# Performance work log

Measured on AMD Instinct MI355X. Metric: run time of the kernel, lower is better.

Reference implementation:

```python
import jax, jax.numpy as jnp
import numpy as np

HIDDEN_DIM = 256
N = 8192


def setup_inputs() -> dict:
    key = jax.random.key(0)
    k1, k2, k3, k4 = jax.random.split(key, 4)
    img = jax.random.normal(k1, (N, HIDDEN_DIM), dtype=jnp.float32)
    text = jax.random.normal(k2, (N, HIDDEN_DIM), dtype=jnp.float32)
    # nn.Linear(hidden_dim, hidden_dim, bias=False) weights, shape [out, in]
    scale = 1.0 / np.sqrt(HIDDEN_DIM)
    Wq = jax.random.uniform(k3, (HIDDEN_DIM, HIDDEN_DIM), dtype=jnp.float32, minval=-scale, maxval=scale)
    Wk = jax.random.uniform(k4, (HIDDEN_DIM, HIDDEN_DIM), dtype=jnp.float32, minval=-scale, maxval=scale)
    return {"img": img, "text": text, "Wq": Wq, "Wk": Wk}


def reference(img, text, Wq, Wk):
    d = img.shape[-1]
    norm_fact = 1.0 / jnp.sqrt(jnp.asarray(d, dtype=img.dtype))
    Q = img @ Wq.T                       # [N, D]
    K = text @ Wk.T                      # [N, D]
    scores = Q @ K.T                     # [N, N]
    # softmax over dim=1 (keys), then scaled by 1/sqrt(D)
    attn = jax.nn.softmax(scores, axis=1) * norm_fact
    out_img = attn @ img                 # [N, D]
    out_text = attn @ text               # [N, D]
    return (out_img, out_text)
```

## Files before the change

### kernel.cpp

```cpp
#include <hip/hip_runtime.h>

typedef unsigned short ushort_t;
typedef unsigned int uint_t;
typedef __attribute__((ext_vector_type(8))) short short8;
typedef __attribute__((ext_vector_type(8))) _Float16 half8;
typedef __attribute__((ext_vector_type(4))) _Float16 half4;
typedef __attribute__((ext_vector_type(4))) float float4v;

#define MFMA_BF16(a, b, c) __builtin_amdgcn_mfma_f32_16x16x32_bf16((a), (b), (c), 0, 0, 0)
#define MFMA_F16(a, b, c) __builtin_amdgcn_mfma_f32_16x16x32_f16((a), (b), (c), 0, 0, 0)

#define NQ 8192
#define DIM 256
#define DV 512

__device__ __forceinline__ ushort_t f2bf(float x) {
  union { float f; uint_t u; } v; v.f = x;
  return (ushort_t)((v.u + 0x7fffu + ((v.u >> 16) & 1u)) >> 16);
}
__device__ __forceinline__ float bf2f(ushort_t b) {
  union { uint_t u; float f; } v; v.u = ((uint_t)b) << 16;
  return v.f;
}

__device__ __forceinline__ half8 cvt8h(const float* p) {
  float4v a = *(const float4v*)p;
  float4v b = *(const float4v*)(p + 4);
  half8 r;
  r[0] = (_Float16)a[0]; r[1] = (_Float16)a[1];
  r[2] = (_Float16)a[2]; r[3] = (_Float16)a[3];
  r[4] = (_Float16)b[0]; r[5] = (_Float16)b[1];
  r[6] = (_Float16)b[2]; r[7] = (_Float16)b[3];
  return r;
}

__device__ __forceinline__ half8 as_h8(short8 s) {
  union { short8 s; half8 h; } u; u.s = s; return u.h;
}

__device__ __forceinline__ void load_lds_16(const void* g, void* l) {
  __builtin_amdgcn_global_load_lds(
      (const __attribute__((address_space(1))) uint_t*)g,
      (__attribute__((address_space(3))) uint_t*)l, 16, 0, 0);
}

__device__ __forceinline__ void barrier_vm0_lgkm0() {
  asm volatile("s_waitcnt vmcnt(0) lgkmcnt(0)\ns_barrier" ::: "memory");
}
__device__ __forceinline__ void barrier_lgkm0() {
  asm volatile("s_waitcnt lgkmcnt(0)\ns_barrier" ::: "memory");
}

__global__ __launch_bounds__(256, 2) void pre_kernel(
    const float* __restrict__ img, const float* __restrict__ text,
    const float* __restrict__ Wq, const float* __restrict__ Wk,
    _Float16* __restrict__ Qh, _Float16* __restrict__ Kh,
    ushort_t* __restrict__ Vt) {
  __shared__ float tile[64][65];
  const int bid = blockIdx.x;
  const int tid = threadIdx.x;
  if (bid < 1024) {
    const int bx = bid & 127;
    const int by = (bid >> 7) & 3;
    const int bz = bid >> 9;
    const int lane = tid & 63;
    const int wv = tid >> 6;
    const int l16 = lane & 15;
    const int quad = lane >> 4;
    const float* A = bz ? text : img;
    const float* W = bz ? Wk : Wq;
    _Float16* C = bz ? Kh : Qh;
    const int row = bx * 64 + wv * 16 + l16;
    const int colbase = by * 64;

    float4v acc[4];
#pragma unroll
    for (int c = 0; c < 4; ++c) acc[c] = (float4v){0.f, 0.f, 0.f, 0.f};
#pragma unroll
    for (int f = 0; f < 8; ++f) {
      const int k0 = f * 32 + quad * 8;
      half8 af = cvt8h(A + (size_t)row * DIM + k0);
#pragma unroll
      for (int c = 0; c < 4; ++c) {
        half8 bfr = cvt8h(W + (size_t)(colbase + c * 16 + l16) * DIM + k0);
        acc[c] = MFMA_F16(af, bfr, acc[c]);
      }
    }
    const int rbase = bx * 64 + wv * 16 + quad * 4;
#pragma unroll
    for (int c = 0; c < 4; ++c)
#pragma unroll
      for (int r = 0; r < 4; ++r)
        C[(size_t)(rbase + r) * DIM + colbase + c * 16 + l16] = (_Float16)acc[c][r];
  } else {
    const int vb = bid - 1024;
    const int n0 = (vb & 127) * 64;
    const int c0 = (vb >> 7) * 64;
    const float* src = (c0 < 256) ? img : text;
    const int cc0 = (c0 < 256) ? c0 : (c0 - 256);
#pragma unroll
    for (int i = 0; i < 4; ++i) {
      const int r = i * 16 + (tid >> 4);
      const int c = (tid & 15) * 4;
      *(float4v*)&tile[r][c] = *(const float4v*)(src + (size_t)(n0 + r) * DIM + cc0 + c);
    }
    __syncthreads();
    const int c = tid >> 2;
    const int seg = tid & 3;
    ushort_t tmp[16];
#pragma unroll
    for (int t = 0; t < 16; ++t) tmp[t] = f2bf(tile[seg * 16 + t][c]);
    ushort_t* dst = Vt + (size_t)(c0 + c) * NQ + n0 + seg * 16;
    *(short8*)dst = *(short8*)&tmp[0];
    *(short8*)(dst + 8) = *(short8*)&tmp[8];
  }
}

__device__ __forceinline__ void stage_K(const _Float16* __restrict__ Kh, int k0,
                                        ushort_t* dst, int tid, int wv) {
#pragma unroll
  for (int i = 0; i < 4; ++i) {
    const int chunk = i * 256 + tid;
    const int n = chunk >> 5;
    const int cs = (chunk & 31) ^ (n & 7);
    load_lds_16(Kh + (size_t)(k0 + n) * DIM + cs * 8,
                (char*)dst + (i * 256 + wv * 64) * 16);
  }
}
__device__ __forceinline__ void stage_V(const ushort_t* __restrict__ Vt, int k0,
                                        ushort_t* dst, int tid, int wv) {
#pragma unroll
  for (int i = 0; i < 8; ++i) {
    const int chunk = i * 256 + tid;
    const int vrow = chunk >> 2;
    const int dc = (chunk & 3) ^ ((vrow >> 1) & 3);
    load_lds_16(Vt + (size_t)vrow * NQ + k0 + dc * 8,
                (char*)dst + (i * 256 + wv * 64) * 16);
  }
}

__global__ __launch_bounds__(256, 2) void attn_kernel(
    const _Float16* __restrict__ Qh, const _Float16* __restrict__ Kh,
    const ushort_t* __restrict__ Vt, _Float16* __restrict__ pacc,
    float* __restrict__ pdenom, int kps, int ks) {
  extern __shared__ __align__(16) ushort_t smem[];
  ushort_t* ldsV = smem + 16384;

  const int tid = threadIdx.x;
  const int lane = tid & 63;
  const int wv = tid >> 6;
  const int l16 = lane & 15;
  const int quad = lane >> 4;
  const int id = blockIdx.x;
  const int split = id & (ks - 1);
  const int qtile = id / ks;
  const int kbeg = split * kps;
  const int sw2 = (l16 >> 1) & 3;
  const int swk = l16 & 7;

  short8 qf[8];
  {
    const _Float16* qptr = Qh + (size_t)(qtile * 64 + wv * 16 + l16) * DIM;
#pragma unroll
    for (int f = 0; f < 8; ++f)
      qf[f] = *(const short8*)(qptr + f * 32 + quad * 8);
  }

  float4v acc[4][8];
#pragma unroll
  for (int m = 0; m < 4; ++m)
#pragma unroll
    for (int c = 0; c < 8; ++c) acc[m][c] = (float4v){0.f, 0.f, 0.f, 0.f};
  float dacc[4] = {0.f, 0.f, 0.f, 0.f};

  const int ntiles = kps >> 5;

  stage_K(Kh, kbeg, smem, tid, wv);
  stage_V(Vt, kbeg, ldsV, tid, wv);

  for (int t = 0; t < ntiles; ++t) {
    const ushort_t* Kt = smem + (t & 1) * 8192;
    barrier_vm0_lgkm0();
    if (t + 1 < ntiles)
      stage_K(Kh, kbeg + (t + 1) * 32, smem + ((t + 1) & 1) * 8192, tid, wv);

    if (t > 0) {
      const ushort_t* Pprev = smem + 32768 + ((t - 1) & 1) * 2048;
      short8 pa[4];
#pragma unroll
      for (int m = 0; m < 4; ++m)
        pa[m] = *(const short8*)(Pprev + (m * 16 + l16) * 32 + (quad ^ sw2) * 8);
#pragma unroll
      for (int c = 0; c < 8; ++c) {
        const int vcol = (wv * 8 + c) * 16 + l16;
        short8 vb = *(const short8*)(ldsV + vcol * 32 + (quad ^ sw2) * 8);
#pragma unroll
        for (int m = 0; m < 4; ++m)
          acc[m][c] = MFMA_BF16(pa[m], vb, acc[m][c]);
      }
    }

    float4v s0 = (float4v){0.f, 0.f, 0.f, 0.f};
    float4v s1 = (float4v){0.f, 0.f, 0.f, 0.f};
#pragma unroll
    for (int f = 0; f < 8; ++f) {
      const int cs = ((f * 4 + quad) ^ swk) * 8;
      short8 kb0 = *(const short8*)(Kt + l16 * DIM + cs);
      short8 kb1 = *(const short8*)(Kt + (l16 + 16) * DIM + cs);
      s0 = MFMA_F16(as_h8(qf[f]), as_h8(kb0), s0);
      s1 = MFMA_F16(as_h8(qf[f]), as_h8(kb1), s1);
    }

    barrier_lgkm0();
    if (t >= 1) stage_V(Vt, kbeg + t * 32, ldsV, tid, wv);

    ushort_t* Pcur = smem + 32768 + (t & 1) * 2048;
    ushort_t pb0[4], pb1[4];
#pragma unroll
    for (int r = 0; r < 4; ++r) {
      pb0[r] = f2bf(__expf(s0[r]));
      pb1[r] = f2bf(__expf(s1[r]));
    }
#pragma unroll
    for (int r = 0; r < 4; ++r) {
      const int rb = wv * 16 + quad * 4 + r;
      const int swp = (rb >> 1) & 3;
      Pcur[rb * 32 + ((l16 >> 3) ^ swp) * 8 + (l16 & 7)] = pb0[r];
      Pcur[rb * 32 + ((2 + (l16 >> 3)) ^ swp) * 8 + (l16 & 7)] = pb1[r];
      dacc[r] += bf2f(pb0[r]) + bf2f(pb1[r]);
    }
  }

  barrier_vm0_lgkm0();
  {
    const ushort_t* Pprev = smem + 32768 + ((ntiles - 1) & 1) * 2048;
    short8 pa[4];
#pragma unroll
    for (int m = 0; m < 4; ++m)
      pa[m] = *(const short8*)(Pprev + (m * 16 + l16) * 32 + (quad ^ sw2) * 8);
#pragma unroll
    for (int c = 0; c < 8; ++c) {
      const int vcol = (wv * 8 + c) * 16 + l16;
      short8 vb = *(const short8*)(ldsV + vcol * 32 + (quad ^ sw2) * 8);
#pragma unroll
      for (int m = 0; m < 4; ++m)
        acc[m][c] = MFMA_BF16(pa[m], vb, acc[m][c]);
    }
  }

#pragma unroll
  for (int r = 0; r < 4; ++r) {
    float ts = dacc[r];
    ts += __shfl_xor(ts, 1);
    ts += __shfl_xor(ts, 2);
    ts += __shfl_xor(ts, 4);
    ts += __shfl_xor(ts, 8);
    dacc[r] = ts;
  }

  barrier_lgkm0();
  float* ldsD = (float*)smem;
  if (l16 == 0) {
#pragma unroll
    for (int r = 0; r < 4; ++r)
      ldsD[wv * 16 + quad * 4 + r] = dacc[r];
  }
  barrier_lgkm0();

  _Float16* pout = pacc + (size_t)split * ((size_t)NQ * DV);
#pragma unroll
  for (int m = 0; m < 4; ++m) {
    float invd[4];
#pragma unroll
    for (int r = 0; r < 4; ++r) invd[r] = 1.0f / ldsD[m * 16 + quad * 4 + r];
    const int rowbase = qtile * 64 + m * 16 + quad * 4;
#pragma unroll
    for (int c = 0; c < 8; ++c) {
      const int col = (wv * 8 + c) * 16 + l16;
#pragma unroll
      for (int r = 0; r < 4; ++r)
        pout[(size_t)(rowbase + r) * DV + col] = (_Float16)(acc[m][c][r] * invd[r]);
    }
  }
  if (l16 == 0) {
    const int rowbase = qtile * 64 + wv * 16 + quad * 4;
#pragma unroll
    for (int r = 0; r < 4; ++r)
      pdenom[split * NQ + rowbase + r] = dacc[r];
  }
}

__global__ __launch_bounds__(256) void combine_kernel(
    const _Float16* __restrict__ pacc, const float* __restrict__ pdenom,
    float* __restrict__ out, int ks) {
  const int idx = blockIdx.x * 256 + threadIdx.x;
  const int n = idx >> 6;
  const int c8 = (idx & 63) << 3;
  float s[8] = {0.f, 0.f, 0.f, 0.f, 0.f, 0.f, 0.f, 0.f};
  float dsum = 0.f;
  for (int sp = 0; sp < ks; ++sp) {
    const float d = pdenom[sp * NQ + n];
    half8 x = *(const half8*)(pacc + (size_t)sp * ((size_t)NQ * DV) + (size_t)n * DV + c8);
#pragma unroll
    for (int j = 0; j < 8; ++j) s[j] += d * (float)x[j];
    dsum += d;
  }
  const float scale = 1.0f / (16.0f * dsum);
  float4v lo = (float4v){s[0], s[1], s[2], s[3]} * scale;
  float4v hi = (float4v){s[4], s[5], s[6], s[7]} * scale;
  float* dst = (c8 < 256) ? (out + (size_t)n * DIM + c8)
                          : (out + (size_t)NQ * DIM + (size_t)n * DIM + (c8 - 256));
  *(float4v*)dst = lo;
  *(float4v*)(dst + 4) = hi;
}

extern "C" void kernel_launch(void* const* d_in, const int* in_sizes, int n_in,
                              void* d_out, int out_size, void* d_ws, size_t ws_size,
                              hipStream_t stream) {
  const float* img = (const float*)d_in[0];
  const float* text = (const float*)d_in[1];
  const float* Wq = (const float*)d_in[2];
  const float* Wk = (const float*)d_in[3];
  float* out = (float*)d_out;
  char* ws = (char*)d_ws;

  _Float16* Qh = (_Float16*)ws;
  _Float16* Kh = (_Float16*)(ws + ((size_t)4 << 20));
  ushort_t* Vt = (ushort_t*)(ws + ((size_t)8 << 20));
  const size_t accsz = (size_t)NQ * DV * sizeof(_Float16);
  const size_t base = (size_t)16 << 20;

  int ks = 4;
  if (ws_size < base + 4 * (accsz + NQ * sizeof(float))) ks = 2;
  _Float16* pacc = (_Float16*)(ws + base);
  float* pdenom = (float*)(ws + base + (size_t)ks * accsz);

  hipLaunchKernelGGL(pre_kernel, dim3(2048), dim3(256), 0, stream,
                     img, text, Wq, Wk, Qh, Kh, Vt);
  hipLaunchKernelGGL(attn_kernel, dim3(128 * ks), dim3(256),
                     36864 * sizeof(ushort_t), stream,
                     Qh, Kh, Vt, pacc, pdenom, NQ / ks, ks);
  hipLaunchKernelGGL(combine_kernel, dim3((NQ * DV / 8) / 256), dim3(256), 0, stream,
                     pacc, pdenom, out, ks);
}
```

Baseline: 244.7 us.

## Pre-convert inputs and weights to fp16; raise MFMA wave priority in attention

Adds a conversion kernel that turns img, text, Wq and Wk into fp16 once, so the projection kernel reads half-precision data directly. Before, it re-converted fp32 weights and activations in every block, and each W row was reloaded by all 128 row-blocks. The projection kernel's launch bounds rise to 4 blocks per SM. The attention kernel also wraps its MFMA loops in s_setprio so the matrix work is favoured during scheduling. The cost is an extra launch and an extra write and read of the fp16 copies through the workspace, which aliases the pacc region.

```diff
diff --git a/kernel.cpp b/kernel.cpp
--- a/kernel.cpp
+++ b/kernel.cpp
@@ -51,11 +51,31 @@
   asm volatile("s_waitcnt lgkmcnt(0)\ns_barrier" ::: "memory");
 }
 
-__global__ __launch_bounds__(256, 2) void pre_kernel(
+__global__ __launch_bounds__(256) void conv_kernel(
     const float* __restrict__ img, const float* __restrict__ text,
     const float* __restrict__ Wq, const float* __restrict__ Wk,
-    _Float16* __restrict__ Qh, _Float16* __restrict__ Kh,
-    ushort_t* __restrict__ Vt) {
+    _Float16* __restrict__ Ah, _Float16* __restrict__ Whq,
+    _Float16* __restrict__ Whk) {
+  const int bid = blockIdx.x;
+  const int tid = threadIdx.x;
+  if (bid < 2048) {
+    const int half = bid >> 10;
+    const size_t off = ((size_t)(bid & 1023) * 256 + tid) * 8;
+    const float* src = half ? text : img;
+    _Float16* dst = Ah + (size_t)half * NQ * DIM + off;
+    *(half8*)dst = cvt8h(src + off);
+  } else {
+    const size_t off = ((size_t)(bid - 2048) * 256 + tid) * 8;
+    *(half8*)(Whq + off) = cvt8h(Wq + off);
+    *(half8*)(Whk + off) = cvt8h(Wk + off);
+  }
+}
+
+__global__ __launch_bounds__(256, 4) void pre_kernel(
+    const float* __restrict__ img, const float* __restrict__ text,
+    const _Float16* __restrict__ Ah, const _Float16* __restrict__ Whq,
+    const _Float16* __restrict__ Whk, _Float16* __restrict__ Qh,
+    _Float16* __restrict__ Kh, ushort_t* __restrict__ Vt) {
   __shared__ float tile[64][65];
   const int bid = blockIdx.x;
   const int tid = threadIdx.x;
@@ -67,8 +87,8 @@
     const int wv = tid >> 6;
     const int l16 = lane & 15;
     const int quad = lane >> 4;
-    const float* A = bz ? text : img;
-    const float* W = bz ? Wk : Wq;
+    const _Float16* A = Ah + (size_t)bz * NQ * DIM;
+    const _Float16* W = bz ? Whk : Whq;
     _Float16* C = bz ? Kh : Qh;
     const int row = bx * 64 + wv * 16 + l16;
     const int colbase = by * 64;
@@ -79,10 +99,10 @@
 #pragma unroll
     for (int f = 0; f < 8; ++f) {
       const int k0 = f * 32 + quad * 8;
-      half8 af = cvt8h(A + (size_t)row * DIM + k0);
+      half8 af = *(const half8*)(A + (size_t)row * DIM + k0);
 #pragma unroll
       for (int c = 0; c < 4; ++c) {
-        half8 bfr = cvt8h(W + (size_t)(colbase + c * 16 + l16) * DIM + k0);
+        half8 bfr = *(const half8*)(W + (size_t)(colbase + c * 16 + l16) * DIM + k0);
         acc[c] = MFMA_F16(af, bfr, acc[c]);
       }
     }
@@ -190,6 +210,7 @@
 #pragma unroll
       for (int m = 0; m < 4; ++m)
         pa[m] = *(const short8*)(Pprev + (m * 16 + l16) * 32 + (quad ^ sw2) * 8);
+      __builtin_amdgcn_s_setprio(1);
 #pragma unroll
       for (int c = 0; c < 8; ++c) {
         const int vcol = (wv * 8 + c) * 16 + l16;
@@ -198,10 +219,12 @@
         for (int m = 0; m < 4; ++m)
           acc[m][c] = MFMA_BF16(pa[m], vb, acc[m][c]);
       }
+      __builtin_amdgcn_s_setprio(0);
     }
 
     float4v s0 = (float4v){0.f, 0.f, 0.f, 0.f};
     float4v s1 = (float4v){0.f, 0.f, 0.f, 0.f};
+    __builtin_amdgcn_s_setprio(1);
 #pragma unroll
     for (int f = 0; f < 8; ++f) {
       const int cs = ((f * 4 + quad) ^ swk) * 8;
@@ -210,6 +233,7 @@
       s0 = MFMA_F16(as_h8(qf[f]), as_h8(kb0), s0);
       s1 = MFMA_F16(as_h8(qf[f]), as_h8(kb1), s1);
     }
+    __builtin_amdgcn_s_setprio(0);
 
     barrier_lgkm0();
     if (t >= 1) stage_V(Vt, kbeg + t * 32, ldsV, tid, wv);
@@ -334,9 +358,14 @@
   if (ws_size < base + 4 * (accsz + NQ * sizeof(float))) ks = 2;
   _Float16* pacc = (_Float16*)(ws + base);
   float* pdenom = (float*)(ws + base + (size_t)ks * accsz);
-
+  _Float16* Ah = (_Float16*)(ws + base);
+  _Float16* Whq = (_Float16*)(ws + base + ((size_t)8 << 20));
+  _Float16* Whk = Whq + DIM * DIM;
+
+  hipLaunchKernelGGL(conv_kernel, dim3(2080), dim3(256), 0, stream,
+                     img, text, Wq, Wk, Ah, Whq, Whk);
   hipLaunchKernelGGL(pre_kernel, dim3(2048), dim3(256), 0, stream,
-                     img, text, Wq, Wk, Qh, Kh, Vt);
+                     img, text, Ah, Whq, Whk, Qh, Kh, Vt);
   hipLaunchKernelGGL(attn_kernel, dim3(128 * ks), dim3(256),
                      36864 * sizeof(ushort_t), stream,
                      Qh, Kh, Vt, pacc, pdenom, NQ / ks, ks);
```

After: 234.0 us. 1.05x faster.
